# Kernel optimization log

Hardware: AMD Instinct MI355X
Metric: run time of the kernel (lower is better)

## Reference

```python
import jax, jax.numpy as jnp
import numpy as np

B, F, K = 65536, 1024, 1024


def setup_inputs() -> dict:
    key = jax.random.key(0)
    kx, kc = jax.random.split(key)
    X = jax.random.normal(kx, (B, F), dtype=jnp.float32)
    # torch.rand init for centroids: uniform [0,1)
    centroids = jax.random.uniform(kc, (K, F), dtype=jnp.float32)
    return {"X": X, "centroids": centroids}


def reference(X, centroids):
    # Squared Euclidean distances via the GEMM expansion; argmin is invariant
    # to sqrt so we skip it (matches torch.argmin(torch.cdist(...)))
    x2 = jnp.sum(X * X, axis=-1, keepdims=True)            # [B,1]
    c2 = jnp.sum(centroids * centroids, axis=-1)           # [K]
    cross = X @ centroids.T                                # [B,K]
    d2 = x2 - 2.0 * cross + c2                             # [B,K]
    return jnp.argmin(d2, axis=1).astype(jnp.int32)
```

## Files before the change

### kernel.cpp

```cpp
#include <hip/hip_runtime.h>


#define NB 65536
#define ND 1024
#define NK 1024
#define BM 32
#define TAU 0.02f
#define BATCH 8

typedef _Float16 f16x8 __attribute__((ext_vector_type(8)));
typedef float f32x16 __attribute__((ext_vector_type(16)));

__device__ __forceinline__ void comb3(float& m1, int& a1, float& m2,
                                      float om1, int oa1, float om2) {
  if (om1 < m1 || (om1 == m1 && oa1 < a1)) {
    m2 = fminf(m1, om2);
    m1 = om1; a1 = oa1;
  } else {
    m2 = fminf(m2, om1);
  }
}

__global__ __launch_bounds__(256) void k_split(const float* __restrict__ cent,
                                               _Float16* __restrict__ chi,
                                               _Float16* __restrict__ clo) {
  const int f8 = blockIdx.x;
#pragma unroll
  for (int rep = 0; rep < 4; ++rep) {
    const int col = rep * 256 + threadIdx.x;
    const float* src = cent + (size_t)col * ND + f8 * 8;
    float4 a = *(const float4*)src;
    float4 b = *(const float4*)(src + 4);
    float xv[8] = {a.x, a.y, a.z, a.w, b.x, b.y, b.z, b.w};
    f16x8 hv, lv;
#pragma unroll
    for (int j = 0; j < 8; ++j) {
      float x = xv[j];
      _Float16 h = (_Float16)x;
      hv[j] = h;
      lv[j] = (_Float16)(x - (float)h);
    }
    *(f16x8*)(chi + ((size_t)f8 * NK + col) * 8) = hv;
    *(f16x8*)(clo + ((size_t)f8 * NK + col) * 8) = lv;
  }
}

__global__ __launch_bounds__(256) void k_c2(const float* __restrict__ cent,
                                            float* __restrict__ c2,
                                            int* __restrict__ cnt) {
  const int col = blockIdx.x;
  const int t = threadIdx.x;
  if (col == 0 && t == 0) *cnt = 0;
  const float* src = cent + (size_t)col * ND;
  float ss = 0.f;
  for (int f = t; f < ND; f += 256) {
    float v = src[f];
    ss = fmaf(v, v, ss);
  }
#pragma unroll
  for (int m = 1; m < 64; m <<= 1) ss += __shfl_xor(ss, m, 64);
  __shared__ float sr[4];
  if ((t & 63) == 0) sr[t >> 6] = ss;
  __syncthreads();
  if (t == 0) c2[col] = sr[0] + sr[1] + sr[2] + sr[3];
}

__global__ __launch_bounds__(256, 3) void k_main(const float* __restrict__ X,
                                                 const _Float16* __restrict__ chi,
                                                 const _Float16* __restrict__ clo,
                                                 const float* __restrict__ c2,
                                                 int* __restrict__ outIdx,
                                                 int* __restrict__ cnt,
                                                 int* __restrict__ list) {
  __shared__ f16x8 Ah[8 * BM];
  __shared__ f16x8 Al[8 * BM];
  __shared__ float pm1[BM][4], pm2[BM][4];
  __shared__ int pa1[BM][4];
  __shared__ float c2s[NK];

  const int tid = threadIdx.x;
  const int lane = tid & 63;
  const int wn = tid >> 6;
  const int lc = lane & 31;
  const int hi = lane >> 5;
  const size_t row0 = (size_t)blockIdx.x * BM;

#pragma unroll
  for (int j = 0; j < 4; ++j) c2s[tid + j * 256] = c2[tid + j * 256];
  if (tid < BM) {
#pragma unroll
    for (int j = 0; j < 4; ++j) {
      pm1[tid][j] = __builtin_inff();
      pm2[tid][j] = __builtin_inff();
      pa1[tid][j] = 0x7fffffff;
    }
  }

  const int ar = tid >> 3;
  const int ak8 = tid & 7;
  const float* xptr = X + (row0 + ar) * (size_t)ND + ak8 * 8;
  const int aslot = ak8 * BM + (ar ^ ak8);

  for (int pass = 0; pass < 2; ++pass) {
    f32x16 acc[4] = {};
    const size_t hb = (((size_t)hi * NK) + pass * 512 + wn * 128 + lc) * 8;
    const _Float16* bh = chi + hb;
    const _Float16* bl = clo + hb;

    float4 ga = *(const float4*)(xptr);
    float4 gb = *(const float4*)(xptr + 4);

    for (int ks = 0; ks < 16; ++ks) {
      __syncthreads();
      {
        float xv[8] = {ga.x, ga.y, ga.z, ga.w, gb.x, gb.y, gb.z, gb.w};
        f16x8 hv, lv;
#pragma unroll
        for (int j = 0; j < 8; ++j) {
          float x = xv[j];
          _Float16 h = (_Float16)x;
          hv[j] = h;
          lv[j] = (_Float16)(x - (float)h);
        }
        Ah[aslot] = hv;
        Al[aslot] = lv;
      }
      if (ks < 15) {
        ga = *(const float4*)(xptr + (ks + 1) * 64);
        gb = *(const float4*)(xptr + (ks + 1) * 64 + 4);
      }
      __syncthreads();

#pragma unroll
      for (int sl = 0; sl < 4; ++sl) {
        const size_t bo = ((size_t)(ks * 8 + sl * 2)) * (NK * 8);
        f16x8 fbh[4], fbl[4], fah, fal;
#pragma unroll
        for (int fn = 0; fn < 4; ++fn) {
          fbh[fn] = *(const f16x8*)(bh + bo + fn * 256);
          fbl[fn] = *(const f16x8*)(bl + bo + fn * 256);
        }
        {
          const int k8 = sl * 2 + hi;
          const int s = k8 * BM + (lc ^ k8);
          fah = Ah[s];
          fal = Al[s];
        }
#pragma unroll
        for (int fn = 0; fn < 4; ++fn)
          acc[fn] = __builtin_amdgcn_mfma_f32_32x32x16_f16(fah, fbh[fn],
                                                           acc[fn], 0, 0, 0);
#pragma unroll
        for (int fn = 0; fn < 4; ++fn)
          acc[fn] = __builtin_amdgcn_mfma_f32_32x32x16_f16(fah, fbl[fn],
                                                           acc[fn], 0, 0, 0);
#pragma unroll
        for (int fn = 0; fn < 4; ++fn)
          acc[fn] = __builtin_amdgcn_mfma_f32_32x32x16_f16(fal, fbh[fn],
                                                           acc[fn], 0, 0, 0);
      }
    }

#pragma unroll
    for (int reg = 0; reg < 16; ++reg) {
      const int orow = (reg & 3) + 8 * (reg >> 2) + 4 * hi;
      float m1 = __builtin_inff(), m2 = __builtin_inff();
      int a1 = 0x7fffffff;
#pragma unroll
      for (int fn = 0; fn < 4; ++fn) {
        const int cg = pass * 512 + wn * 128 + fn * 32 + lc;
        const float v = c2s[cg] - 2.0f * acc[fn][reg];
        if (v < m1 || (v == m1 && cg < a1)) {
          m2 = m1; m1 = v; a1 = cg;
        } else {
          m2 = fminf(m2, v);
        }
      }
#pragma unroll
      for (int mk = 1; mk < 32; mk <<= 1) {
        float om1 = __shfl_xor(m1, mk, 64);
        float om2 = __shfl_xor(m2, mk, 64);
        int oa1 = __shfl_xor(a1, mk, 64);
        comb3(m1, a1, m2, om1, oa1, om2);
      }
      if (lc == 0) {
        float rm1 = pm1[orow][wn], rm2 = pm2[orow][wn];
        int ra1 = pa1[orow][wn];
        comb3(rm1, ra1, rm2, m1, a1, m2);
        pm1[orow][wn] = rm1;
        pm2[orow][wn] = rm2;
        pa1[orow][wn] = ra1;
      }
    }
  }
  __syncthreads();
  if (tid < BM) {
    float m1 = pm1[tid][0], m2 = pm2[tid][0];
    int a1 = pa1[tid][0];
#pragma unroll
    for (int j = 1; j < 4; ++j)
      comb3(m1, a1, m2, pm1[tid][j], pa1[tid][j], pm2[tid][j]);
    outIdx[row0 + tid] = a1;
    if (!(m2 - m1 > TAU)) {
      int k = atomicAdd(cnt, 1);
      list[k] = (int)(row0 + tid);
    }
  }
}

__global__ __launch_bounds__(256) void k_rescue(const float* __restrict__ X,
                                                const float* __restrict__ cent,
                                                const int* __restrict__ cnt,
                                                const int* __restrict__ list,
                                                int* __restrict__ outIdx) {
  __shared__ float4 xs4[BATCH][ND / 4];
  __shared__ int rows_s[BATCH];
  __shared__ double x2p[BATCH][4];
  __shared__ double rmw[BATCH][4];
  __shared__ int raw_[BATCH][4];
  const int t = threadIdx.x;
  const int lane = t & 63, wv = t >> 6;
  const int count = *cnt;

  for (int chunk = blockIdx.x; chunk * BATCH < count; chunk += 256) {
    const int n = min(BATCH, count - chunk * BATCH);
    __syncthreads();
    if (t < n) rows_s[t] = list[chunk * BATCH + t];
    __syncthreads();
#pragma unroll
    for (int r = 0; r < BATCH; ++r)
      if (r < n) xs4[r][t] = ((const float4*)(X + (size_t)rows_s[r] * ND))[t];
    __syncthreads();
#pragma unroll
    for (int r = 0; r < BATCH; ++r) {
      float4 v = xs4[r][t];
      double ss = (double)v.x * v.x + (double)v.y * v.y +
                  (double)v.z * v.z + (double)v.w * v.w;
#pragma unroll
      for (int mk = 1; mk < 64; mk <<= 1) ss += __shfl_xor(ss, mk, 64);
      if (lane == 0) x2p[r][wv] = ss;
    }
    __syncthreads();
    double dt[4][BATCH] = {};
    double c2d[4] = {};
    const float* cp0 = cent + (size_t)t * ND;
    for (int f = 0; f < ND; f += 4) {
      float4 cv[4];
#pragma unroll
      for (int j = 0; j < 4; ++j)
        cv[j] = *(const float4*)(cp0 + (size_t)j * 256 * ND + f);
#pragma unroll
      for (int j = 0; j < 4; ++j)
        c2d[j] += (double)cv[j].x * cv[j].x + (double)cv[j].y * cv[j].y +
                  (double)cv[j].z * cv[j].z + (double)cv[j].w * cv[j].w;
#pragma unroll
      for (int r = 0; r < BATCH; ++r) {
        float4 xv = xs4[r][f >> 2];
#pragma unroll
        for (int j = 0; j < 4; ++j) {
          dt[j][r] += (double)xv.x * cv[j].x + (double)xv.y * cv[j].y +
                      (double)xv.z * cv[j].z + (double)xv.w * cv[j].w;
        }
      }
    }
#pragma unroll
    for (int r = 0; r < BATCH; ++r) {
      const double x2 = x2p[r][0] + x2p[r][1] + x2p[r][2] + x2p[r][3];
      double bm = __builtin_inf();
      int ba = 0x7fffffff;
#pragma unroll
      for (int j = 0; j < 4; ++j) {
        const int c = t + j * 256;
        const double d2 = x2 - 2.0 * dt[j][r] + c2d[j];
        if (d2 < bm || (d2 == bm && c < ba)) { bm = d2; ba = c; }
      }
#pragma unroll
      for (int mk = 1; mk < 64; mk <<= 1) {
        double ob = __shfl_xor(bm, mk, 64);
        int oa = __shfl_xor(ba, mk, 64);
        if (ob < bm || (ob == bm && oa < ba)) { bm = ob; ba = oa; }
      }
      if (lane == 0) { rmw[r][wv] = bm; raw_[r][wv] = ba; }
    }
    __syncthreads();
    if (t < n) {
      double fb = rmw[t][0];
      int fa = raw_[t][0];
#pragma unroll
      for (int j = 1; j < 4; ++j)
        if (rmw[t][j] < fb || (rmw[t][j] == fb && raw_[t][j] < fa)) {
          fb = rmw[t][j]; fa = raw_[t][j];
        }
      outIdx[rows_s[t]] = fa;
    }
  }
}

__global__ __launch_bounds__(256) void k_naive(const float* __restrict__ X,
                                               const float* __restrict__ cent,
                                               int* __restrict__ outIdx) {
  __shared__ float4 xs4[ND / 4];
  __shared__ float rbm[4];
  __shared__ int rba[4];
  const int row = blockIdx.x;
  const int t = threadIdx.x;
  const int lane = t & 63, wv = t >> 6;
  xs4[t] = ((const float4*)(X + (size_t)row * ND))[t];
  __syncthreads();
  const float* xs = (const float*)xs4;
  float bm = __builtin_inff();
  int ba = 0x7fffffff;
  for (int c = t; c < NK; c += 256) {
    const float* cp = cent + (size_t)c * ND;
    float s = 0.f;
#pragma unroll 4
    for (int f = 0; f < ND; f += 4) {
      float4 cv = *(const float4*)(cp + f);
      float d0 = xs[f] - cv.x, d1 = xs[f + 1] - cv.y;
      float d2_ = xs[f + 2] - cv.z, d3 = xs[f + 3] - cv.w;
      s = fmaf(d0, d0, s); s = fmaf(d1, d1, s);
      s = fmaf(d2_, d2_, s); s = fmaf(d3, d3, s);
    }
    if (s < bm || (s == bm && c < ba)) { bm = s; ba = c; }
  }
#pragma unroll
  for (int mk = 1; mk < 64; mk <<= 1) {
    float ob = __shfl_xor(bm, mk, 64);
    int oa = __shfl_xor(ba, mk, 64);
    if (ob < bm || (ob == bm && oa < ba)) { bm = ob; ba = oa; }
  }
  if (lane == 0) { rbm[wv] = bm; rba[wv] = ba; }
  __syncthreads();
  if (t == 0) {
    float fb = rbm[0];
    int fa = rba[0];
#pragma unroll
    for (int j = 1; j < 4; ++j)
      if (rbm[j] < fb || (rbm[j] == fb && rba[j] < fa)) { fb = rbm[j]; fa = rba[j]; }
    outIdx[row] = fa;
  }
}

extern "C" void kernel_launch(void* const* d_in, const int* in_sizes, int n_in,
                              void* d_out, int out_size, void* d_ws, size_t ws_size,
                              hipStream_t stream) {
  const float* X = (const float*)d_in[0];
  const float* cent = (const float*)d_in[1];
  int* outIdx = (int*)d_out;

  const size_t WS_NEEDED = (4u << 20) + (64u << 10) + (1u << 10) + (256u << 10);
  if (ws_size < WS_NEEDED) {
    k_naive<<<dim3(NB), dim3(256), 0, stream>>>(X, cent, outIdx);
    return;
  }
  char* ws = (char*)d_ws;
  _Float16* chi = (_Float16*)ws;
  _Float16* clo = (_Float16*)(ws + (2u << 20));
  float* c2 = (float*)(ws + (4u << 20));
  int* cnt = (int*)(ws + (4u << 20) + (64u << 10));
  int* list = (int*)(ws + (4u << 20) + (64u << 10) + (1u << 10));

  k_split<<<dim3(ND / 8), dim3(256), 0, stream>>>(cent, chi, clo);
  k_c2<<<dim3(NK), dim3(256), 0, stream>>>(cent, c2, cnt);
  k_main<<<dim3(NB / BM), dim3(256), 0, stream>>>(X, chi, clo, c2, outIdx, cnt, list);
  k_rescue<<<dim3(256), dim3(256), 0, stream>>>(X, cent, cnt, list, outIdx);
}
```

Measured before the change: 1.011 ms.

## Drop split-fp16 GEMM for single fp16 MFMA with wider rescue margin

The main kernel stops using the three-MFMA hi/lo fp16 split and computes the cross term with a single fp16 product, which cuts MFMA work per tile to a third and removes the low-part centroid buffer. To absorb the larger rounding error, the ambiguity margin TAU is raised so more rows fall into the exact fp64 rescue pass. The rescue grid doubles and hoists the centroid-norm computation out of its chunk loop. The row tile grows to 64 with a double-buffered LDS A tile and one barrier per k-step. The risk is a much larger rescue list, since its cost depends on how many rows land within the margin.

Result: faster. 961.4 us (-4.9%).

```diff
diff --git a/kernel.cpp b/kernel.cpp
--- a/kernel.cpp
+++ b/kernel.cpp
@@ -4,9 +4,10 @@
 #define NB 65536
 #define ND 1024
 #define NK 1024
-#define BM 32
-#define TAU 0.02f
+#define BM 64
+#define TAU 0.15f
 #define BATCH 8
+#define RGRID 512
 
 typedef _Float16 f16x8 __attribute__((ext_vector_type(8)));
 typedef float f32x16 __attribute__((ext_vector_type(16)));
@@ -22,8 +23,7 @@
 }
 
 __global__ __launch_bounds__(256) void k_split(const float* __restrict__ cent,
-                                               _Float16* __restrict__ chi,
-                                               _Float16* __restrict__ clo) {
+                                               _Float16* __restrict__ chi) {
   const int f8 = blockIdx.x;
 #pragma unroll
   for (int rep = 0; rep < 4; ++rep) {
@@ -32,16 +32,10 @@
     float4 a = *(const float4*)src;
     float4 b = *(const float4*)(src + 4);
     float xv[8] = {a.x, a.y, a.z, a.w, b.x, b.y, b.z, b.w};
-    f16x8 hv, lv;
-#pragma unroll
-    for (int j = 0; j < 8; ++j) {
-      float x = xv[j];
-      _Float16 h = (_Float16)x;
-      hv[j] = h;
-      lv[j] = (_Float16)(x - (float)h);
-    }
+    f16x8 hv;
+#pragma unroll
+    for (int j = 0; j < 8; ++j) hv[j] = (_Float16)xv[j];
     *(f16x8*)(chi + ((size_t)f8 * NK + col) * 8) = hv;
-    *(f16x8*)(clo + ((size_t)f8 * NK + col) * 8) = lv;
   }
 }
 
@@ -65,15 +59,13 @@
   if (t == 0) c2[col] = sr[0] + sr[1] + sr[2] + sr[3];
 }
 
-__global__ __launch_bounds__(256, 3) void k_main(const float* __restrict__ X,
+__global__ __launch_bounds__(256, 2) void k_main(const float* __restrict__ X,
                                                  const _Float16* __restrict__ chi,
-                                                 const _Float16* __restrict__ clo,
                                                  const float* __restrict__ c2,
                                                  int* __restrict__ outIdx,
                                                  int* __restrict__ cnt,
                                                  int* __restrict__ list) {
-  __shared__ f16x8 Ah[8 * BM];
-  __shared__ f16x8 Al[8 * BM];
+  __shared__ f16x8 Abuf[2][8 * BM];
   __shared__ float pm1[BM][4], pm2[BM][4];
   __shared__ int pa1[BM][4];
   __shared__ float c2s[NK];
@@ -87,109 +79,115 @@
 
 #pragma unroll
   for (int j = 0; j < 4; ++j) c2s[tid + j * 256] = c2[tid + j * 256];
-  if (tid < BM) {
-#pragma unroll
-    for (int j = 0; j < 4; ++j) {
-      pm1[tid][j] = __builtin_inff();
-      pm2[tid][j] = __builtin_inff();
-      pa1[tid][j] = 0x7fffffff;
-    }
-  }
-
-  const int ar = tid >> 3;
+  ((float*)pm1)[tid] = __builtin_inff();
+  ((float*)pm2)[tid] = __builtin_inff();
+  ((int*)pa1)[tid] = 0x7fffffff;
+
+  const int ar0 = tid >> 3;
   const int ak8 = tid & 7;
-  const float* xptr = X + (row0 + ar) * (size_t)ND + ak8 * 8;
-  const int aslot = ak8 * BM + (ar ^ ak8);
+  const float* xptr = X + (row0 + ar0) * (size_t)ND + ak8 * 8;
+  const int slot0 = ak8 * BM + (ar0 ^ ak8);
+  const int slot1 = ak8 * BM + ((ar0 + 32) ^ ak8);
 
   for (int pass = 0; pass < 2; ++pass) {
-    f32x16 acc[4] = {};
-    const size_t hb = (((size_t)hi * NK) + pass * 512 + wn * 128 + lc) * 8;
-    const _Float16* bh = chi + hb;
-    const _Float16* bl = clo + hb;
-
-    float4 ga = *(const float4*)(xptr);
-    float4 gb = *(const float4*)(xptr + 4);
+    f32x16 acc[2][4] = {};
+    const _Float16* bh =
+        chi + (((size_t)hi * NK) + pass * 512 + wn * 128 + lc) * 8;
+
+    {
+      float4 ga0 = *(const float4*)(xptr);
+      float4 gb0 = *(const float4*)(xptr + 4);
+      float4 ga1 = *(const float4*)(xptr + 32 * ND);
+      float4 gb1 = *(const float4*)(xptr + 32 * ND + 4);
+      float x0[8] = {ga0.x, ga0.y, ga0.z, ga0.w, gb0.x, gb0.y, gb0.z, gb0.w};
+      float x1[8] = {ga1.x, ga1.y, ga1.z, ga1.w, gb1.x, gb1.y, gb1.z, gb1.w};
+      f16x8 h0, h1;
+#pragma unroll
+      for (int j = 0; j < 8; ++j) {
+        h0[j] = (_Float16)x0[j];
+        h1[j] = (_Float16)x1[j];
+      }
+      Abuf[0][slot0] = h0;
+      Abuf[0][slot1] = h1;
+    }
+    __syncthreads();
 
     for (int ks = 0; ks < 16; ++ks) {
-      __syncthreads();
-      {
-        float xv[8] = {ga.x, ga.y, ga.z, ga.w, gb.x, gb.y, gb.z, gb.w};
-        f16x8 hv, lv;
-#pragma unroll
-        for (int j = 0; j < 8; ++j) {
-          float x = xv[j];
-          _Float16 h = (_Float16)x;
-          hv[j] = h;
-          lv[j] = (_Float16)(x - (float)h);
-        }
-        Ah[aslot] = hv;
-        Al[aslot] = lv;
-      }
+      const int cur = ks & 1;
+      float4 ga0, gb0, ga1, gb1;
       if (ks < 15) {
-        ga = *(const float4*)(xptr + (ks + 1) * 64);
-        gb = *(const float4*)(xptr + (ks + 1) * 64 + 4);
-      }
-      __syncthreads();
-
+        ga0 = *(const float4*)(xptr + (ks + 1) * 64);
+        gb0 = *(const float4*)(xptr + (ks + 1) * 64 + 4);
+        ga1 = *(const float4*)(xptr + 32 * ND + (ks + 1) * 64);
+        gb1 = *(const float4*)(xptr + 32 * ND + (ks + 1) * 64 + 4);
+      }
 #pragma unroll
       for (int sl = 0; sl < 4; ++sl) {
         const size_t bo = ((size_t)(ks * 8 + sl * 2)) * (NK * 8);
-        f16x8 fbh[4], fbl[4], fah, fal;
-#pragma unroll
-        for (int fn = 0; fn < 4; ++fn) {
+        f16x8 fbh[4], fah[2];
+#pragma unroll
+        for (int fn = 0; fn < 4; ++fn)
           fbh[fn] = *(const f16x8*)(bh + bo + fn * 256);
-          fbl[fn] = *(const f16x8*)(bl + bo + fn * 256);
-        }
         {
           const int k8 = sl * 2 + hi;
-          const int s = k8 * BM + (lc ^ k8);
-          fah = Ah[s];
-          fal = Al[s];
-        }
-#pragma unroll
-        for (int fn = 0; fn < 4; ++fn)
-          acc[fn] = __builtin_amdgcn_mfma_f32_32x32x16_f16(fah, fbh[fn],
-                                                           acc[fn], 0, 0, 0);
-#pragma unroll
-        for (int fn = 0; fn < 4; ++fn)
-          acc[fn] = __builtin_amdgcn_mfma_f32_32x32x16_f16(fah, fbl[fn],
-                                                           acc[fn], 0, 0, 0);
-#pragma unroll
-        for (int fn = 0; fn < 4; ++fn)
-          acc[fn] = __builtin_amdgcn_mfma_f32_32x32x16_f16(fal, fbh[fn],
-                                                           acc[fn], 0, 0, 0);
-      }
-    }
-
-#pragma unroll
-    for (int reg = 0; reg < 16; ++reg) {
-      const int orow = (reg & 3) + 8 * (reg >> 2) + 4 * hi;
-      float m1 = __builtin_inff(), m2 = __builtin_inff();
-      int a1 = 0x7fffffff;
-#pragma unroll
-      for (int fn = 0; fn < 4; ++fn) {
-        const int cg = pass * 512 + wn * 128 + fn * 32 + lc;
-        const float v = c2s[cg] - 2.0f * acc[fn][reg];
-        if (v < m1 || (v == m1 && cg < a1)) {
-          m2 = m1; m1 = v; a1 = cg;
-        } else {
-          m2 = fminf(m2, v);
-        }
-      }
-#pragma unroll
-      for (int mk = 1; mk < 32; mk <<= 1) {
-        float om1 = __shfl_xor(m1, mk, 64);
-        float om2 = __shfl_xor(m2, mk, 64);
-        int oa1 = __shfl_xor(a1, mk, 64);
-        comb3(m1, a1, m2, om1, oa1, om2);
-      }
-      if (lc == 0) {
-        float rm1 = pm1[orow][wn], rm2 = pm2[orow][wn];
-        int ra1 = pa1[orow][wn];
-        comb3(rm1, ra1, rm2, m1, a1, m2);
-        pm1[orow][wn] = rm1;
-        pm2[orow][wn] = rm2;
-        pa1[orow][wn] = ra1;
+#pragma unroll
+          for (int fm = 0; fm < 2; ++fm)
+            fah[fm] = Abuf[cur][k8 * BM + ((fm * 32 + lc) ^ k8)];
+        }
+#pragma unroll
+        for (int fm = 0; fm < 2; ++fm)
+#pragma unroll
+          for (int fn = 0; fn < 4; ++fn)
+            acc[fm][fn] = __builtin_amdgcn_mfma_f32_32x32x16_f16(
+                fah[fm], fbh[fn], acc[fm][fn], 0, 0, 0);
+      }
+      if (ks < 15) {
+        float x0[8] = {ga0.x, ga0.y, ga0.z, ga0.w, gb0.x, gb0.y, gb0.z, gb0.w};
+        float x1[8] = {ga1.x, ga1.y, ga1.z, ga1.w, gb1.x, gb1.y, gb1.z, gb1.w};
+        f16x8 h0, h1;
+#pragma unroll
+        for (int j = 0; j < 8; ++j) {
+          h0[j] = (_Float16)x0[j];
+          h1[j] = (_Float16)x1[j];
+        }
+        Abuf[cur ^ 1][slot0] = h0;
+        Abuf[cur ^ 1][slot1] = h1;
+        __syncthreads();
+      }
+    }
+
+#pragma unroll
+    for (int fm = 0; fm < 2; ++fm) {
+#pragma unroll
+      for (int reg = 0; reg < 16; ++reg) {
+        const int orow = fm * 32 + (reg & 3) + 8 * (reg >> 2) + 4 * hi;
+        float m1 = __builtin_inff(), m2 = __builtin_inff();
+        int a1 = 0x7fffffff;
+#pragma unroll
+        for (int fn = 0; fn < 4; ++fn) {
+          const int cg = pass * 512 + wn * 128 + fn * 32 + lc;
+          const float v = c2s[cg] - 2.0f * acc[fm][fn][reg];
+          if (v < m1 || (v == m1 && cg < a1)) {
+            m2 = m1; m1 = v; a1 = cg;
+          } else {
+            m2 = fminf(m2, v);
+          }
+        }
+#pragma unroll
+        for (int mk = 1; mk < 32; mk <<= 1) {
+          float om1 = __shfl_xor(m1, mk, 64);
+          float om2 = __shfl_xor(m2, mk, 64);
+          int oa1 = __shfl_xor(a1, mk, 64);
+          comb3(m1, a1, m2, om1, oa1, om2);
+        }
+        if (lc == 0) {
+          float rm1 = pm1[orow][wn], rm2 = pm2[orow][wn];
+          int ra1 = pa1[orow][wn];
+          comb3(rm1, ra1, rm2, m1, a1, m2);
+          pm1[orow][wn] = rm1;
+          pm2[orow][wn] = rm2;
+          pa1[orow][wn] = ra1;
+        }
       }
     }
   }
@@ -213,6 +211,9 @@
                                                 const int* __restrict__ cnt,
                                                 const int* __restrict__ list,
                                                 int* __restrict__ outIdx) {
+  const int count = *cnt;
+  if (blockIdx.x * BATCH >= count) return;
+
   __shared__ float4 xs4[BATCH][ND / 4];
   __shared__ int rows_s[BATCH];
   __shared__ double x2p[BATCH][4];
@@ -220,9 +221,21 @@
   __shared__ int raw_[BATCH][4];
   const int t = threadIdx.x;
   const int lane = t & 63, wv = t >> 6;
-  const int count = *cnt;
-
-  for (int chunk = blockIdx.x; chunk * BATCH < count; chunk += 256) {
+  const float* cp0 = cent + (size_t)t * ND;
+
+  double c2d[4] = {};
+  for (int f = 0; f < ND; f += 4) {
+    float4 cv[4];
+#pragma unroll
+    for (int j = 0; j < 4; ++j)
+      cv[j] = *(const float4*)(cp0 + (size_t)j * 256 * ND + f);
+#pragma unroll
+    for (int j = 0; j < 4; ++j)
+      c2d[j] += (double)cv[j].x * cv[j].x + (double)cv[j].y * cv[j].y +
+                (double)cv[j].z * cv[j].z + (double)cv[j].w * cv[j].w;
+  }
+
+  for (int chunk = blockIdx.x; chunk * BATCH < count; chunk += RGRID) {
     const int n = min(BATCH, count - chunk * BATCH);
     __syncthreads();
     if (t < n) rows_s[t] = list[chunk * BATCH + t];
@@ -242,17 +255,11 @@
     }
     __syncthreads();
     double dt[4][BATCH] = {};
-    double c2d[4] = {};
-    const float* cp0 = cent + (size_t)t * ND;
     for (int f = 0; f < ND; f += 4) {
       float4 cv[4];
 #pragma unroll
       for (int j = 0; j < 4; ++j)
         cv[j] = *(const float4*)(cp0 + (size_t)j * 256 * ND + f);
-#pragma unroll
-      for (int j = 0; j < 4; ++j)
-        c2d[j] += (double)cv[j].x * cv[j].x + (double)cv[j].y * cv[j].y +
-                  (double)cv[j].z * cv[j].z + (double)cv[j].w * cv[j].w;
 #pragma unroll
       for (int r = 0; r < BATCH; ++r) {
         float4 xv = xs4[r][f >> 2];
@@ -348,20 +355,19 @@
   const float* cent = (const float*)d_in[1];
   int* outIdx = (int*)d_out;
 
-  const size_t WS_NEEDED = (4u << 20) + (64u << 10) + (1u << 10) + (256u << 10);
+  const size_t WS_NEEDED = (2u << 20) + (64u << 10) + (1u << 10) + (256u << 10);
   if (ws_size < WS_NEEDED) {
     k_naive<<<dim3(NB), dim3(256), 0, stream>>>(X, cent, outIdx);
     return;
   }
   char* ws = (char*)d_ws;
   _Float16* chi = (_Float16*)ws;
-  _Float16* clo = (_Float16*)(ws + (2u << 20));
-  float* c2 = (float*)(ws + (4u << 20));
-  int* cnt = (int*)(ws + (4u << 20) + (64u << 10));
-  int* list = (int*)(ws + (4u << 20) + (64u << 10) + (1u << 10));
-
-  k_split<<<dim3(ND / 8), dim3(256), 0, stream>>>(cent, chi, clo);
+  float* c2 = (float*)(ws + (2u << 20));
+  int* cnt = (int*)(ws + (2u << 20) + (64u << 10));
+  int* list = (int*)(ws + (2u << 20) + (64u << 10) + (1u << 10));
+
+  k_split<<<dim3(ND / 8), dim3(256), 0, stream>>>(cent, chi);
   k_c2<<<dim3(NK), dim3(256), 0, stream>>>(cent, c2, cnt);
-  k_main<<<dim3(NB / BM), dim3(256), 0, stream>>>(X, chi, clo, c2, outIdx, cnt, list);
-  k_rescue<<<dim3(256), dim3(256), 0, stream>>>(X, cent, cnt, list, outIdx);
-}
+  k_main<<<dim3(NB / BM), dim3(256), 0, stream>>>(X, chi, c2, outIdx, cnt, list);
+  k_rescue<<<dim3(RGRID), dim3(256), 0, stream>>>(X, cent, cnt, list, outIdx);
+}
```
